# Performance work log

Measured on AMD Instinct MI355X. Metric: run time of the kernel, lower is better.

## Reference

```python
import jax, jax.numpy as jnp
import numpy as np

MAX_DISP = 10
KS = 2 * MAX_DISP + 1  # 21 -> 441 displacements


def setup_inputs() -> dict:
    key = jax.random.key(0)
    k1, k2 = jax.random.split(key)
    B, C, H, W = 4, 64, 128, 128
    feat1 = jax.random.normal(k1, (B, C, H, W), dtype=jnp.float32)
    feat2 = jax.random.normal(k2, (B, C, H, W), dtype=jnp.float32)
    return {"feat1": feat1, "feat2": feat2}


def _correlation(feat1, feat2):
    B, C, H, W = feat1.shape
    pad = MAX_DISP
    feat2_p = jnp.pad(feat2, ((0, 0), (0, 0), (pad, pad), (pad, pad)))

    # all (i, j) displacements, flattened row-major to match torch cat order
    ii, jj = jnp.meshgrid(jnp.arange(KS), jnp.arange(KS), indexing="ij")
    shifts = jnp.stack([ii.ravel(), jj.ravel()], axis=-1)  # [KS*KS, 2]

    def one_shift(ij):
        i, j = ij[0], ij[1]
        f2 = jax.lax.dynamic_slice(feat2_p, (0, 0, i, j), (B, C, H, W))
        # reduce over channel dim only; avoid materializing product per-shift
        return jnp.einsum("bchw,bchw->bhw", feat1, f2) / C

    corr = jax.vmap(one_shift)(shifts)            # [KS*KS, B, H, W]
    return jnp.transpose(corr, (1, 0, 2, 3))      # [B, KS*KS, H, W]


def reference(feat1, feat2):
    return _correlation(feat1, feat2)
```

## Files before the change

### kernel.cpp

```cpp
#include <hip/hip_runtime.h>

#define BB  4
#define CC  64
#define HH  128
#define WW  128
#define KS  21
#define PAD 10

__global__ __launch_bounds__(256) void corr_kernel(
    const float* __restrict__ feat1,
    const float* __restrict__ feat2,
    float* __restrict__ out)
{
    const int tid = threadIdx.x;
    int bi = blockIdx.x;
    const int di = bi % KS;  bi /= KS;
    const int h8 = bi % (HH / 8);
    const int b  = bi / (HH / 8);

    const int h  = h8 * 8 + (tid >> 5);
    const int w0 = (tid & 31) << 2;

    const int r = h + di - PAD;

    float acc[4][KS];
#pragma unroll
    for (int p = 0; p < 4; ++p)
#pragma unroll
        for (int d = 0; d < KS; ++d) acc[p][d] = 0.0f;

    if (r >= 0 && r < HH) {
        const float* f1p = feat1 + ((size_t)(b * CC) * HH + h) * WW + w0;
        const float* f2p = feat2 + ((size_t)(b * CC) * HH + r) * WW;

#pragma unroll 2
        for (int c = 0; c < CC; ++c) {
            const float4 a = *(const float4*)(f1p + (size_t)c * (HH * WW));

            float win[28];
#pragma unroll
            for (int j = 0; j < 7; ++j) {
                const int off = w0 - 12 + 4 * j;
                float4 v = make_float4(0.f, 0.f, 0.f, 0.f);
                if (off >= 0 && off < WW)
                    v = *(const float4*)(f2p + (size_t)c * (HH * WW) + off);
                win[4 * j + 0] = v.x;
                win[4 * j + 1] = v.y;
                win[4 * j + 2] = v.z;
                win[4 * j + 3] = v.w;
            }

#pragma unroll
            for (int d = 0; d < KS; ++d) {
                acc[0][d] += a.x * win[d + 2];
                acc[1][d] += a.y * win[d + 3];
                acc[2][d] += a.z * win[d + 4];
                acc[3][d] += a.w * win[d + 5];
            }
        }
    }

    const float scale = 1.0f / (float)CC;
    float* op = out + (((size_t)b * (KS * KS) + (size_t)di * KS) * HH + h) * WW + w0;
#pragma unroll
    for (int d = 0; d < KS; ++d) {
        float4 v = make_float4(acc[0][d] * scale, acc[1][d] * scale,
                               acc[2][d] * scale, acc[3][d] * scale);
        *(float4*)(op + (size_t)d * (HH * WW)) = v;
    }
}

extern "C" void kernel_launch(void* const* d_in, const int* in_sizes, int n_in,
                              void* d_out, int out_size, void* d_ws, size_t ws_size,
                              hipStream_t stream) {
    const float* feat1 = (const float*)d_in[0];
    const float* feat2 = (const float*)d_in[1];
    float* out = (float*)d_out;

    const int blocks = BB * (HH / 8) * KS;
    corr_kernel<<<blocks, 256, 0, stream>>>(feat1, feat2, out);
}
```

Before: 229.7 us.

## Stage feat2 rows through shared memory with zero-padded halo per channel chunk

Each block now copies its 8 shifted feat2 rows for 4 channels at a time into shared memory, with zeroed halo columns. Threads then read their 28-wide window from shared memory instead of issuing 7 global float4 loads each, which removes redundant global loads and the per-load bounds branches. Launch bounds now request 3 blocks per SM. In exchange it adds two barriers per chunk and runs the full compute even for out-of-range rows (it multiplies zeros), and the register cap may cause spills for the 84 accumulators.

```diff
diff --git a/kernel.cpp b/kernel.cpp
--- a/kernel.cpp
+++ b/kernel.cpp
@@ -6,22 +6,41 @@
 #define WW  128
 #define KS  21
 #define PAD 10
+#define CH  4
+#define LROW 160
 
-__global__ __launch_bounds__(256) void corr_kernel(
+__global__ __launch_bounds__(256, 3) void corr_kernel(
     const float* __restrict__ feat1,
     const float* __restrict__ feat2,
     float* __restrict__ out)
 {
+    __shared__ float lds[CH * 8 * LROW];
+
     const int tid = threadIdx.x;
     int bi = blockIdx.x;
     const int di = bi % KS;  bi /= KS;
     const int h8 = bi % (HH / 8);
     const int b  = bi / (HH / 8);
 
+    {
+        const int rr = tid >> 3;
+        const int q  = tid & 7;
+        const int col = (q < 4) ? (q << 2) : (144 + ((q - 4) << 2));
+        *(float4*)&lds[rr * LROW + col] = make_float4(0.f, 0.f, 0.f, 0.f);
+    }
+
     const int h  = h8 * 8 + (tid >> 5);
     const int w0 = (tid & 31) << 2;
+    const int r0 = h8 * 8 + di - PAD;
 
-    const int r = h + di - PAD;
+    const int s_q   = tid & 31;
+    const int s_row = (tid >> 5) & 7;
+    const int sr    = r0 + s_row;
+    const bool s_ok = (sr >= 0) && (sr < HH);
+    const float* f2p = feat2 + ((size_t)(b * CC) * HH + (s_ok ? sr : 0)) * WW + (s_q << 2);
+    float* ldst = &lds[s_row * LROW + 16 + (s_q << 2)];
+
+    const float* f1p = feat1 + ((size_t)(b * CC) * HH + h) * WW + w0;
 
     float acc[4][KS];
 #pragma unroll
@@ -29,27 +48,30 @@
 #pragma unroll
         for (int d = 0; d < KS; ++d) acc[p][d] = 0.0f;
 
-    if (r >= 0 && r < HH) {
-        const float* f1p = feat1 + ((size_t)(b * CC) * HH + h) * WW + w0;
-        const float* f2p = feat2 + ((size_t)(b * CC) * HH + r) * WW;
+    for (int c0 = 0; c0 < CC; c0 += CH) {
+        __syncthreads();
+#pragma unroll
+        for (int cl = 0; cl < CH; ++cl) {
+            float4 v = make_float4(0.f, 0.f, 0.f, 0.f);
+            if (s_ok)
+                v = *(const float4*)(f2p + (size_t)(c0 + cl) * (HH * WW));
+            *(float4*)(ldst + cl * (8 * LROW)) = v;
+        }
+        __syncthreads();
 
-#pragma unroll 2
-        for (int c = 0; c < CC; ++c) {
-            const float4 a = *(const float4*)(f1p + (size_t)c * (HH * WW));
-
+#pragma unroll
+        for (int cl = 0; cl < CH; ++cl) {
+            const float4 a = *(const float4*)(f1p + (size_t)(c0 + cl) * (HH * WW));
+            const float* wp = &lds[(cl * 8 + (tid >> 5)) * LROW + 4 + w0];
             float win[28];
 #pragma unroll
             for (int j = 0; j < 7; ++j) {
-                const int off = w0 - 12 + 4 * j;
-                float4 v = make_float4(0.f, 0.f, 0.f, 0.f);
-                if (off >= 0 && off < WW)
-                    v = *(const float4*)(f2p + (size_t)c * (HH * WW) + off);
-                win[4 * j + 0] = v.x;
-                win[4 * j + 1] = v.y;
-                win[4 * j + 2] = v.z;
-                win[4 * j + 3] = v.w;
+                const float4 t = *(const float4*)(wp + (j << 2));
+                win[4 * j + 0] = t.x;
+                win[4 * j + 1] = t.y;
+                win[4 * j + 2] = t.z;
+                win[4 * j + 3] = t.w;
             }
-
 #pragma unroll
             for (int d = 0; d < KS; ++d) {
                 acc[0][d] += a.x * win[d + 2];
```

Measured after the change: 259.7 us. +13.1%, slower.

## Compute correlation with split-bf16 MFMA over channel-last padded copies

Applied to the files above, without the earlier changes.

Adds prep kernels that transpose feat1 and a padded feat2 to channel-last layout and split each value into hi/lo bf16 parts. The main kernel then computes the correlation with 16x16x32 bf16 MFMA tiles, using three products (hh, lh, hl) to approximate fp32 accuracy. The aim is to move the channel reduction from scalar FMAs onto the matrix cores. The cost is extra workspace traffic for the prep passes, a scattered scalar output store, wasted MFMA work outside the displacement band, and a small precision loss from dropping the lo*lo term. A fallback to the old kernel runs when the workspace is too small.

```diff
diff --git a/kernel.cpp b/kernel.cpp
--- a/kernel.cpp
+++ b/kernel.cpp
@@ -1,42 +1,172 @@
 #include <hip/hip_runtime.h>
 
-#define BB  4
-#define CC  64
-#define HH  128
-#define WW  128
-#define KS  21
+typedef short bf16x8 __attribute__((ext_vector_type(8)));
+typedef float f32x4 __attribute__((ext_vector_type(4)));
+
+#define BB 4
+#define CC 64
+#define HH 128
+#define WW 128
+#define KS 21
 #define PAD 10
 
-__global__ __launch_bounds__(256) void corr_kernel(
-    const float* __restrict__ feat1,
-    const float* __restrict__ feat2,
-    float* __restrict__ out)
-{
+#define RR 148
+#define VV 160
+
+#define A_ELEMS ((size_t)BB * HH * WW * CC)
+#define B_ELEMS ((size_t)BB * RR * VV * CC)
+#define WS_NEED ((2 * A_ELEMS + 2 * B_ELEMS) * 2)
+
+__device__ inline ushort f2bf(float x) {
+    uint u = __float_as_uint(x);
+    return (ushort)((u + 0x7FFFu + ((u >> 16) & 1u)) >> 16);
+}
+__device__ inline float bf2f(ushort h) { return __uint_as_float(((uint)h) << 16); }
+
+__global__ __launch_bounds__(256) void prep_a(const float* __restrict__ f1,
+                                              ushort* __restrict__ Ah,
+                                              ushort* __restrict__ Al) {
+    const int idx = blockIdx.x * 256 + threadIdx.x;
+    const int b = idx >> 14, hw = idx & 16383;
+    const float* src = f1 + (size_t)b * (CC * HH * WW) + hw;
+    ushort* dh = Ah + (size_t)idx * CC;
+    ushort* dl = Al + (size_t)idx * CC;
+#pragma unroll
+    for (int k8 = 0; k8 < 8; ++k8) {
+        bf16x8 vh, vl;
+#pragma unroll
+        for (int j = 0; j < 8; ++j) {
+            float x = src[(size_t)(k8 * 8 + j) * (HH * WW)];
+            ushort h16 = f2bf(x);
+            vh[j] = (short)h16;
+            vl[j] = (short)f2bf(x - bf2f(h16));
+        }
+        *(bf16x8*)(dh + k8 * 8) = vh;
+        *(bf16x8*)(dl + k8 * 8) = vl;
+    }
+}
+
+__global__ __launch_bounds__(256) void prep_b(const float* __restrict__ f2,
+                                              ushort* __restrict__ Bh,
+                                              ushort* __restrict__ Bl) {
+    const int idx = blockIdx.x * 256 + threadIdx.x;
+    const int vv = idx % VV;
+    const int t  = idx / VV;
+    const int rr = t % RR;
+    const int b  = t / RR;
+    const int r = rr - PAD, wc = vv - PAD;
+    const bool ok = ((unsigned)r < HH) && ((unsigned)wc < WW);
+    const float* src = f2 + ((size_t)(b * CC) * HH + (ok ? r : 0)) * WW + (ok ? wc : 0);
+    ushort* dh = Bh + (size_t)idx * CC;
+    ushort* dl = Bl + (size_t)idx * CC;
+#pragma unroll
+    for (int k8 = 0; k8 < 8; ++k8) {
+        bf16x8 vh, vl;
+#pragma unroll
+        for (int j = 0; j < 8; ++j) {
+            float x = ok ? src[(size_t)(k8 * 8 + j) * (HH * WW)] : 0.0f;
+            ushort h16 = f2bf(x);
+            vh[j] = (short)h16;
+            vl[j] = (short)f2bf(x - bf2f(h16));
+        }
+        *(bf16x8*)(dh + k8 * 8) = vh;
+        *(bf16x8*)(dl + k8 * 8) = vl;
+    }
+}
+
+__global__ __launch_bounds__(256) void corr_mfma(const ushort* __restrict__ Ah,
+                                                 const ushort* __restrict__ Al,
+                                                 const ushort* __restrict__ Bh,
+                                                 const ushort* __restrict__ Bl,
+                                                 float* __restrict__ out) {
+    const int lane = threadIdx.x & 63;
+    const int blk = blockIdx.x;
+    const int e = (blk & 7) * 672 + (blk >> 3);
+    const int wid = e * 4 + (threadIdx.x >> 6);
+    const int grp = wid / 672;
+    const int wi  = wid % 672;
+    const int b = grp >> 3, hc = grp & 7;
+    const int half = wi & 1;
+    const int t2 = wi >> 1;
+    const int di  = t2 % 21;
+    const int h   = hc * 16 + t2 / 21;
+
+    const int i0 = half * 4;
+    const int n  = lane & 15;
+    const int kq = lane >> 4;
+
+    const size_t abase = (((size_t)(b * HH + h)) * WW + (i0 * 16 + n)) * CC + kq * 8;
+    bf16x8 aH[4][2], aL[4][2];
+#pragma unroll
+    for (int ii = 0; ii < 4; ++ii)
+#pragma unroll
+        for (int q = 0; q < 2; ++q) {
+            const size_t off = abase + (size_t)ii * (16 * CC) + q * 32;
+            aH[ii][q] = *(const bf16x8*)(Ah + off);
+            aL[ii][q] = *(const bf16x8*)(Al + off);
+        }
+
+    const int rr = h + di;
+    const size_t bbase = (((size_t)(b * RR + rr)) * VV + n) * CC + kq * 8;
+    const size_t obase = ((size_t)b * (KS * KS) + (size_t)di * KS) * (HH * WW) + (size_t)h * WW;
+    const float inv = 1.0f / (float)CC;
+
+#pragma unroll
+    for (int jt = 0; jt < 6; ++jt) {
+        const int jj = i0 + jt;
+        bf16x8 bH[2], bL[2];
+#pragma unroll
+        for (int q = 0; q < 2; ++q) {
+            const size_t off = bbase + (size_t)jj * (16 * CC) + q * 32;
+            bH[q] = *(const bf16x8*)(Bh + off);
+            bL[q] = *(const bf16x8*)(Bl + off);
+        }
+        const int ilo = (jt < 2) ? 0 : jt - 2;
+        const int ihi = (jt < 3) ? jt : 3;
+#pragma unroll
+        for (int ir = 0; ir < 4; ++ir) {
+            if (ir < ilo || ir > ihi) continue;
+            f32x4 acc = {0.f, 0.f, 0.f, 0.f};
+            acc = __builtin_amdgcn_mfma_f32_16x16x32_bf16(aH[ir][0], bH[0], acc, 0, 0, 0);
+            acc = __builtin_amdgcn_mfma_f32_16x16x32_bf16(aH[ir][1], bH[1], acc, 0, 0, 0);
+            acc = __builtin_amdgcn_mfma_f32_16x16x32_bf16(aL[ir][0], bH[0], acc, 0, 0, 0);
+            acc = __builtin_amdgcn_mfma_f32_16x16x32_bf16(aL[ir][1], bH[1], acc, 0, 0, 0);
+            acc = __builtin_amdgcn_mfma_f32_16x16x32_bf16(aH[ir][0], bL[0], acc, 0, 0, 0);
+            acc = __builtin_amdgcn_mfma_f32_16x16x32_bf16(aH[ir][1], bL[1], acc, 0, 0, 0);
+            const int i = i0 + ir;
+#pragma unroll
+            for (int reg = 0; reg < 4; ++reg) {
+                const int mm = kq * 4 + reg;
+                const int w  = i * 16 + mm;
+                const int dj = (jj - i) * 16 + n - mm;
+                if (dj >= 0 && dj < KS)
+                    out[obase + (size_t)dj * (HH * WW) + w] = acc[reg] * inv;
+            }
+        }
+    }
+}
+
+__global__ __launch_bounds__(256) void corr_fallback(
+    const float* __restrict__ feat1, const float* __restrict__ feat2,
+    float* __restrict__ out) {
     const int tid = threadIdx.x;
     int bi = blockIdx.x;
     const int di = bi % KS;  bi /= KS;
     const int h8 = bi % (HH / 8);
     const int b  = bi / (HH / 8);
-
     const int h  = h8 * 8 + (tid >> 5);
     const int w0 = (tid & 31) << 2;
-
     const int r = h + di - PAD;
-
     float acc[4][KS];
 #pragma unroll
     for (int p = 0; p < 4; ++p)
 #pragma unroll
         for (int d = 0; d < KS; ++d) acc[p][d] = 0.0f;
-
     if (r >= 0 && r < HH) {
         const float* f1p = feat1 + ((size_t)(b * CC) * HH + h) * WW + w0;
         const float* f2p = feat2 + ((size_t)(b * CC) * HH + r) * WW;
-
-#pragma unroll 2
         for (int c = 0; c < CC; ++c) {
             const float4 a = *(const float4*)(f1p + (size_t)c * (HH * WW));
-
             float win[28];
 #pragma unroll
             for (int j = 0; j < 7; ++j) {
@@ -44,12 +174,8 @@
                 float4 v = make_float4(0.f, 0.f, 0.f, 0.f);
                 if (off >= 0 && off < WW)
                     v = *(const float4*)(f2p + (size_t)c * (HH * WW) + off);
-                win[4 * j + 0] = v.x;
-                win[4 * j + 1] = v.y;
-                win[4 * j + 2] = v.z;
-                win[4 * j + 3] = v.w;
+                win[4*j] = v.x; win[4*j+1] = v.y; win[4*j+2] = v.z; win[4*j+3] = v.w;
             }
-
 #pragma unroll
             for (int d = 0; d < KS; ++d) {
                 acc[0][d] += a.x * win[d + 2];
@@ -59,13 +185,11 @@
             }
         }
     }
-
     const float scale = 1.0f / (float)CC;
     float* op = out + (((size_t)b * (KS * KS) + (size_t)di * KS) * HH + h) * WW + w0;
 #pragma unroll
     for (int d = 0; d < KS; ++d) {
-        float4 v = make_float4(acc[0][d] * scale, acc[1][d] * scale,
-                               acc[2][d] * scale, acc[3][d] * scale);
+        float4 v = make_float4(acc[0][d]*scale, acc[1][d]*scale, acc[2][d]*scale, acc[3][d]*scale);
         *(float4*)(op + (size_t)d * (HH * WW)) = v;
     }
 }
@@ -77,6 +201,17 @@
     const float* feat2 = (const float*)d_in[1];
     float* out = (float*)d_out;
 
-    const int blocks = BB * (HH / 8) * KS;
-    corr_kernel<<<blocks, 256, 0, stream>>>(feat1, feat2, out);
-}
+    if (ws_size < WS_NEED) {
+        corr_fallback<<<BB * (HH / 8) * KS, 256, 0, stream>>>(feat1, feat2, out);
+        return;
+    }
+
+    ushort* Ah = (ushort*)d_ws;
+    ushort* Al = Ah + A_ELEMS;
+    ushort* Bh = Al + A_ELEMS;
+    ushort* Bl = Bh + B_ELEMS;
+
+    prep_a<<<(BB * HH * WW) / 256, 256, 0, stream>>>(feat1, Ah, Al);
+    prep_b<<<(BB * RR * VV) / 256, 256, 0, stream>>>(feat2, Bh, Bl);
+    corr_mfma<<<5376, 256, 0, stream>>>(Ah, Al, Bh, Bl, out);
+}
```

After: 288.6 us. +25.7%, slower.
